# Performance work log

Hardware: AMD Instinct MI355X
Metric: run time of the kernel (lower is better)

Reference implementation:

```python
import jax, jax.numpy as jnp
import numpy as np


def setup_inputs() -> dict:
    key = jax.random.key(0)
    k1, k2 = jax.random.split(key)
    B, S, D, T = 64, 512, 768, 384
    hidden_states = jax.random.normal(k1, (B, S, D), dtype=jnp.float32)
    # sorted per-row segment ids: each subtoken belongs to a token index in [0, T)
    segment_ids = jnp.sort(jax.random.randint(k2, (B, S), 0, T), axis=-1)
    return {"hidden_states": hidden_states, "segment_ids": segment_ids, "num_tokens": T}


def reference(hidden_states, segment_ids, num_tokens):
    # Segment-mean of subtoken embeddings into token embeddings.
    # Equivalent to the original running-mean loop:
    #   prev + (next - prev) / n_subtoken_per_token  == mean over the group.
    B, S, D = hidden_states.shape
    # flatten batch into segment ids so one segment_sum handles all sequences
    flat_ids = (segment_ids + jnp.arange(B, dtype=segment_ids.dtype)[:, None] * num_tokens).reshape(-1)
    sums = jax.ops.segment_sum(hidden_states.reshape(-1, D), flat_ids,
                               num_segments=B * num_tokens)  # [B*T, D]
    counts = jax.ops.segment_sum(jnp.ones((B * S,), dtype=hidden_states.dtype), flat_ids,
                                 num_segments=B * num_tokens)  # [B*T]
    # tokens with no subtokens stay zero (original initializes with zeros)
    means = sums / jnp.maximum(counts, 1.0)[:, None]
    return means.reshape(B, num_tokens, D)
```

## Files before the change

kernel.cpp:

```cpp
#include <hip/hip_runtime.h>


__global__ void bounds_kernel(const int* __restrict__ seg,
                              const int* __restrict__ num_tokens_p,
                              int* __restrict__ start,
                              int BS_total,
                              int BT) {
  const int T = num_tokens_p[0];
  const int B = BT / T;
  const int S = BS_total / B;
  int idx = blockIdx.x * blockDim.x + threadIdx.x;
  if (idx >= BS_total) return;
  const int b = idx / S;
  const int s = idx - b * S;
  const int cur = seg[idx];
  const int prev = (s == 0) ? -1 : seg[idx - 1];
  int* __restrict__ row = start + (size_t)b * (T + 1);
  for (int t = prev + 1; t <= cur; ++t) row[t] = s;
  if (s == S - 1) {
    for (int t = cur + 1; t <= T; ++t) row[t] = S;
  }
}

__global__ void __launch_bounds__(192) seg_mean_kernel(
    const float* __restrict__ hs,
    const int* __restrict__ start,
    const int* __restrict__ num_tokens_p,
    float* __restrict__ out,
    int BS_total,
    int D) {
  const int T = num_tokens_p[0];
  const int BT = gridDim.x;
  const int S = (int)(((long long)BS_total * T) / BT);
  const int b = blockIdx.x / T;
  const int t = blockIdx.x - b * T;

  const int* __restrict__ srow = start + (size_t)b * (T + 1) + t;
  const int lo = srow[0];
  const int hi = srow[1];
  const int cnt = hi - lo;

  const int d4 = threadIdx.x;
  const int rowstride4 = D >> 2;

  const float4* __restrict__ p =
      (const float4*)(hs + ((size_t)b * S + lo) * D) + d4;

  float4 acc = make_float4(0.f, 0.f, 0.f, 0.f);
  for (int s = 0; s < cnt; ++s) {
    float4 v = p[(size_t)s * rowstride4];
    acc.x += v.x; acc.y += v.y; acc.z += v.z; acc.w += v.w;
  }

  const float inv = (cnt > 0) ? (1.0f / (float)cnt) : 0.0f;
  float4 o = make_float4(acc.x * inv, acc.y * inv, acc.z * inv, acc.w * inv);

  ((float4*)(out + (size_t)blockIdx.x * D))[d4] = o;
}

__global__ void __launch_bounds__(192) seg_mean_search_kernel(
    const float* __restrict__ hs,
    const int* __restrict__ seg,
    const int* __restrict__ num_tokens_p,
    float* __restrict__ out,
    int BS_total,
    int D) {
  const int T = num_tokens_p[0];
  const int BT = gridDim.x;
  const int S = (int)(((long long)BS_total * T) / BT);
  const int b = blockIdx.x / T;
  const int t = blockIdx.x - b * T;
  const int* __restrict__ row = seg + (size_t)b * S;

  int lo = 0, n = S;
  while (n > 0) {
    int half = n >> 1;
    int mid = lo + half;
    if (row[mid] < t) { lo = mid + 1; n -= half + 1; } else { n = half; }
  }
  int hi = lo; n = S - lo;
  while (n > 0) {
    int half = n >> 1;
    int mid = hi + half;
    if (row[mid] < t + 1) { hi = mid + 1; n -= half + 1; } else { n = half; }
  }
  const int cnt = hi - lo;

  const int d4 = threadIdx.x;
  const int rowstride4 = D >> 2;
  const float4* __restrict__ p =
      (const float4*)(hs + ((size_t)b * S + lo) * D) + d4;

  float4 acc = make_float4(0.f, 0.f, 0.f, 0.f);
  for (int s = 0; s < cnt; ++s) {
    float4 v = p[(size_t)s * rowstride4];
    acc.x += v.x; acc.y += v.y; acc.z += v.z; acc.w += v.w;
  }
  const float inv = (cnt > 0) ? (1.0f / (float)cnt) : 0.0f;
  float4 o = make_float4(acc.x * inv, acc.y * inv, acc.z * inv, acc.w * inv);
  ((float4*)(out + (size_t)blockIdx.x * D))[d4] = o;
}

extern "C" void kernel_launch(void* const* d_in, const int* in_sizes, int n_in,
                              void* d_out, int out_size, void* d_ws, size_t ws_size,
                              hipStream_t stream) {
  const float* hs = (const float*)d_in[0];
  const int* seg = (const int*)d_in[1];
  const int* num_tokens_p = (const int*)d_in[2];
  float* out = (float*)d_out;

  const int BS_total = in_sizes[1];
  const int D = in_sizes[0] / in_sizes[1];
  const int BT = out_size / D;

  const size_t ws_needed = (size_t)4 * ((size_t)BT + (size_t)BS_total);

  if (ws_size >= ws_needed) {
    int* start = (int*)d_ws;
    const int threads1 = 256;
    const int grid1 = (BS_total + threads1 - 1) / threads1;
    hipLaunchKernelGGL(bounds_kernel, dim3(grid1), dim3(threads1), 0, stream,
                       seg, num_tokens_p, start, BS_total, BT);
    hipLaunchKernelGGL(seg_mean_kernel, dim3(BT), dim3(D / 4), 0, stream,
                       hs, start, num_tokens_p, out, BS_total, D);
  } else {
    hipLaunchKernelGGL(seg_mean_search_kernel, dim3(BT), dim3(D / 4), 0, stream,
                       hs, seg, num_tokens_p, out, BS_total, D);
  }
}
```

Before: 172.1 us.

## Fuse segment bounds computation into mean kernel with 8 tokens per block

Replaces the separate bounds kernel and per-token mean kernel with a single kernel in which each block handles 8 consecutive tokens. Each block scans its row of segment ids in shared memory, using ballots and atomics to find its start offset and per-token counts, then averages the subtoken rows for each token. This removes one kernel launch and the workspace round trip. In exchange every block rereads a full 512-entry segment row, the grid shrinks by a factor of 8, and each block's token loop runs serially.

Result: slower. 183.1 us (+6.4%).

```diff
diff --git a/kernel.cpp b/kernel.cpp
--- a/kernel.cpp
+++ b/kernel.cpp
@@ -1,104 +1,120 @@
 #include <hip/hip_runtime.h>
 
 
-__global__ void bounds_kernel(const int* __restrict__ seg,
-                              const int* __restrict__ num_tokens_p,
-                              int* __restrict__ start,
-                              int BS_total,
-                              int BT) {
+#define TPB_TOKENS 8
+
+__global__ void __launch_bounds__(192) seg_mean_fused(
+    const float* __restrict__ hs,
+    const int*   __restrict__ seg,
+    const int*   __restrict__ num_tokens_p,
+    float*       __restrict__ out,
+    int BS_total,
+    int BT,
+    int D) {
   const int T = num_tokens_p[0];
   const int B = BT / T;
   const int S = BS_total / B;
-  int idx = blockIdx.x * blockDim.x + threadIdx.x;
-  if (idx >= BS_total) return;
-  const int b = idx / S;
-  const int s = idx - b * S;
-  const int cur = seg[idx];
-  const int prev = (s == 0) ? -1 : seg[idx - 1];
-  int* __restrict__ row = start + (size_t)b * (T + 1);
-  for (int t = prev + 1; t <= cur; ++t) row[t] = s;
-  if (s == S - 1) {
-    for (int t = cur + 1; t <= T; ++t) row[t] = S;
-  }
-}
 
-__global__ void __launch_bounds__(192) seg_mean_kernel(
-    const float* __restrict__ hs,
-    const int* __restrict__ start,
-    const int* __restrict__ num_tokens_p,
-    float* __restrict__ out,
-    int BS_total,
-    int D) {
-  const int T = num_tokens_p[0];
-  const int BT = gridDim.x;
-  const int S = (int)(((long long)BS_total * T) / BT);
-  const int b = blockIdx.x / T;
-  const int t = blockIdx.x - b * T;
+  const int g0 = blockIdx.x * TPB_TOKENS;
+  if (g0 >= BT) return;
+  const int gEnd = min(g0 + TPB_TOKENS, BT);
 
-  const int* __restrict__ srow = start + (size_t)b * (T + 1) + t;
-  const int lo = srow[0];
-  const int hi = srow[1];
-  const int cnt = hi - lo;
-
-  const int d4 = threadIdx.x;
+  const int tid  = threadIdx.x;
+  const int lane = tid & 63;
+  const int d4   = tid;
   const int rowstride4 = D >> 2;
 
-  const float4* __restrict__ p =
-      (const float4*)(hs + ((size_t)b * S + lo) * D) + d4;
+  __shared__ int sh_bounds[TPB_TOKENS + 1];
+  __shared__ int sh_bins[TPB_TOKENS];
+  __shared__ int sh_base;
+  __shared__ int sh_hi;
 
-  float4 acc = make_float4(0.f, 0.f, 0.f, 0.f);
-  for (int s = 0; s < cnt; ++s) {
-    float4 v = p[(size_t)s * rowstride4];
-    acc.x += v.x; acc.y += v.y; acc.z += v.z; acc.w += v.w;
+  const int b0    = g0 / T;
+  const int bLast = (gEnd - 1) / T;
+
+  if (b0 == bLast) {
+    const int t0   = g0 - b0 * T;
+    const int nTok = gEnd - g0;
+
+    if (tid < TPB_TOKENS) sh_bins[tid] = 0;
+    if (tid == 0) sh_base = 0;
+    __syncthreads();
+
+    const int* __restrict__ srow = seg + (size_t)b0 * S;
+    for (int s = tid; s < S; s += blockDim.x) {
+      const int v = srow[s];
+      unsigned long long m = __ballot(v < t0);
+      if (lane == 0) atomicAdd(&sh_base, __popcll(m));
+      const int rel = v - t0;
+      if (rel >= 0 && rel < nTok) atomicAdd(&sh_bins[rel], 1);
+    }
+    __syncthreads();
+
+    if (tid == 0) {
+      int acc = sh_base;
+      sh_bounds[0] = acc;
+      #pragma unroll
+      for (int j = 0; j < TPB_TOKENS; ++j) {
+        acc += sh_bins[j];
+        sh_bounds[j + 1] = acc;
+      }
+    }
+    __syncthreads();
+
+    const float4* __restrict__ base =
+        (const float4*)(hs + (size_t)b0 * S * D) + d4;
+
+    for (int j = 0; j < nTok; ++j) {
+      const int lo  = sh_bounds[j];
+      const int cnt = sh_bounds[j + 1] - lo;
+
+      float4 acc = make_float4(0.f, 0.f, 0.f, 0.f);
+      const float4* __restrict__ p = base + (size_t)lo * rowstride4;
+      for (int s = 0; s < cnt; ++s) {
+        float4 v = p[(size_t)s * rowstride4];
+        acc.x += v.x; acc.y += v.y; acc.z += v.z; acc.w += v.w;
+      }
+      const float inv = (cnt > 0) ? (1.0f / (float)cnt) : 0.0f;
+      float4 o = make_float4(acc.x * inv, acc.y * inv, acc.z * inv, acc.w * inv);
+      ((float4*)(out + (size_t)(g0 + j) * D))[d4] = o;
+    }
+  } else {
+    for (int g = g0; g < gEnd; ++g) {
+      const int b = g / T;
+      const int t = g - b * T;
+
+      if (tid == 0) { sh_base = 0; sh_hi = 0; }
+      __syncthreads();
+
+      const int* __restrict__ srow = seg + (size_t)b * S;
+      for (int s = tid; s < S; s += blockDim.x) {
+        const int v = srow[s];
+        unsigned long long mlo = __ballot(v < t);
+        unsigned long long mhi = __ballot(v < t + 1);
+        if (lane == 0) {
+          atomicAdd(&sh_base, __popcll(mlo));
+          atomicAdd(&sh_hi,   __popcll(mhi));
+        }
+      }
+      __syncthreads();
+
+      const int lo  = sh_base;
+      const int cnt = sh_hi - lo;
+
+      float4 acc = make_float4(0.f, 0.f, 0.f, 0.f);
+      const float4* __restrict__ p =
+          (const float4*)(hs + ((size_t)b * S + lo) * D) + d4;
+      for (int s = 0; s < cnt; ++s) {
+        float4 v = p[(size_t)s * rowstride4];
+        acc.x += v.x; acc.y += v.y; acc.z += v.z; acc.w += v.w;
+      }
+      const float inv = (cnt > 0) ? (1.0f / (float)cnt) : 0.0f;
+      float4 o = make_float4(acc.x * inv, acc.y * inv, acc.z * inv, acc.w * inv);
+      ((float4*)(out + (size_t)g * D))[d4] = o;
+
+      __syncthreads();
+    }
   }
-
-  const float inv = (cnt > 0) ? (1.0f / (float)cnt) : 0.0f;
-  float4 o = make_float4(acc.x * inv, acc.y * inv, acc.z * inv, acc.w * inv);
-
-  ((float4*)(out + (size_t)blockIdx.x * D))[d4] = o;
-}
-
-__global__ void __launch_bounds__(192) seg_mean_search_kernel(
-    const float* __restrict__ hs,
-    const int* __restrict__ seg,
-    const int* __restrict__ num_tokens_p,
-    float* __restrict__ out,
-    int BS_total,
-    int D) {
-  const int T = num_tokens_p[0];
-  const int BT = gridDim.x;
-  const int S = (int)(((long long)BS_total * T) / BT);
-  const int b = blockIdx.x / T;
-  const int t = blockIdx.x - b * T;
-  const int* __restrict__ row = seg + (size_t)b * S;
-
-  int lo = 0, n = S;
-  while (n > 0) {
-    int half = n >> 1;
-    int mid = lo + half;
-    if (row[mid] < t) { lo = mid + 1; n -= half + 1; } else { n = half; }
-  }
-  int hi = lo; n = S - lo;
-  while (n > 0) {
-    int half = n >> 1;
-    int mid = hi + half;
-    if (row[mid] < t + 1) { hi = mid + 1; n -= half + 1; } else { n = half; }
-  }
-  const int cnt = hi - lo;
-
-  const int d4 = threadIdx.x;
-  const int rowstride4 = D >> 2;
-  const float4* __restrict__ p =
-      (const float4*)(hs + ((size_t)b * S + lo) * D) + d4;
-
-  float4 acc = make_float4(0.f, 0.f, 0.f, 0.f);
-  for (int s = 0; s < cnt; ++s) {
-    float4 v = p[(size_t)s * rowstride4];
-    acc.x += v.x; acc.y += v.y; acc.z += v.z; acc.w += v.w;
-  }
-  const float inv = (cnt > 0) ? (1.0f / (float)cnt) : 0.0f;
-  float4 o = make_float4(acc.x * inv, acc.y * inv, acc.z * inv, acc.w * inv);
-  ((float4*)(out + (size_t)blockIdx.x * D))[d4] = o;
 }
 
 extern "C" void kernel_launch(void* const* d_in, const int* in_sizes, int n_in,
@@ -113,18 +129,7 @@
   const int D = in_sizes[0] / in_sizes[1];
   const int BT = out_size / D;
 
-  const size_t ws_needed = (size_t)4 * ((size_t)BT + (size_t)BS_total);
-
-  if (ws_size >= ws_needed) {
-    int* start = (int*)d_ws;
-    const int threads1 = 256;
-    const int grid1 = (BS_total + threads1 - 1) / threads1;
-    hipLaunchKernelGGL(bounds_kernel, dim3(grid1), dim3(threads1), 0, stream,
-                       seg, num_tokens_p, start, BS_total, BT);
-    hipLaunchKernelGGL(seg_mean_kernel, dim3(BT), dim3(D / 4), 0, stream,
-                       hs, start, num_tokens_p, out, BS_total, D);
-  } else {
-    hipLaunchKernelGGL(seg_mean_search_kernel, dim3(BT), dim3(D / 4), 0, stream,
-                       hs, seg, num_tokens_p, out, BS_total, D);
-  }
+  const int grid = (BT + TPB_TOKENS - 1) / TPB_TOKENS;
+  hipLaunchKernelGGL(seg_mean_fused, dim3(grid), dim3(D / 4), 0, stream,
+                     hs, seg, num_tokens_p, out, BS_total, BT, D);
 }
```

## Map one wave per token with grid-stride loop and prefetched absolute bounds

Applied to the files above, without the earlier changes.

The bounds kernel now writes absolute (start,end) row pairs per token instead of per-row start offsets, so the mean kernel needs a single int2 load. The mean kernel assigns one 64-lane wave per token, with each lane handling three float4 columns for D=768. It uses a capped grid-stride loop that prefetches the next token's bounds. This is meant to cut per-block launch and scheduling overhead and raise memory-level parallelism per thread. The cost is fewer resident blocks and a specialised path that only applies when D is 768.

New measurement: 178.0 us. 1.03x slower.

```diff
diff --git a/kernel.cpp b/kernel.cpp
--- a/kernel.cpp
+++ b/kernel.cpp
@@ -1,61 +1,110 @@
 #include <hip/hip_runtime.h>
 
 
-__global__ void bounds_kernel(const int* __restrict__ seg,
-                              const int* __restrict__ num_tokens_p,
-                              int* __restrict__ start,
-                              int BS_total,
-                              int BT) {
+#define PHASE2_WAVES 4
+
+__global__ void bounds_pairs_kernel(const int* __restrict__ seg,
+                                    const int* __restrict__ num_tokens_p,
+                                    int2* __restrict__ pairs,
+                                    int BS_total,
+                                    int BT) {
   const int T = num_tokens_p[0];
   const int B = BT / T;
   const int S = BS_total / B;
-  int idx = blockIdx.x * blockDim.x + threadIdx.x;
+  const int idx = blockIdx.x * blockDim.x + threadIdx.x;
   if (idx >= BS_total) return;
   const int b = idx / S;
   const int s = idx - b * S;
   const int cur = seg[idx];
   const int prev = (s == 0) ? -1 : seg[idx - 1];
-  int* __restrict__ row = start + (size_t)b * (T + 1);
-  for (int t = prev + 1; t <= cur; ++t) row[t] = s;
+  int2* __restrict__ prow = pairs + (size_t)b * T;
+
+  for (int t = prev + 1; t <= cur; ++t) {
+    prow[t].x = idx;
+    if (t > 0) prow[t - 1].y = idx;
+  }
   if (s == S - 1) {
-    for (int t = cur + 1; t <= T; ++t) row[t] = S;
+    const int end = b * S + S;
+    for (int t = cur + 1; t <= T; ++t) {
+      if (t < T) prow[t].x = end;
+      prow[t - 1].y = end;
+    }
   }
 }
 
-__global__ void __launch_bounds__(192) seg_mean_kernel(
+__global__ void __launch_bounds__(64 * PHASE2_WAVES) seg_mean_d768(
     const float* __restrict__ hs,
-    const int* __restrict__ start,
-    const int* __restrict__ num_tokens_p,
-    float* __restrict__ out,
-    int BS_total,
-    int D) {
-  const int T = num_tokens_p[0];
-  const int BT = gridDim.x;
-  const int S = (int)(((long long)BS_total * T) / BT);
-  const int b = blockIdx.x / T;
-  const int t = blockIdx.x - b * T;
+    const int2*  __restrict__ pairs,
+    float*       __restrict__ out,
+    int BT) {
+  const int wave = threadIdx.x >> 6;
+  const int lane = threadIdx.x & 63;
+  const int gstride = gridDim.x * PHASE2_WAVES;
 
-  const int* __restrict__ srow = start + (size_t)b * (T + 1) + t;
-  const int lo = srow[0];
-  const int hi = srow[1];
-  const int cnt = hi - lo;
+  int g = blockIdx.x * PHASE2_WAVES + wave;
+  if (g >= BT) return;
+  int2 lh = pairs[g];
 
-  const int d4 = threadIdx.x;
-  const int rowstride4 = D >> 2;
+  while (true) {
+    const int gn = g + gstride;
+    int2 lh_next;
+    if (gn < BT) lh_next = pairs[gn];
 
-  const float4* __restrict__ p =
-      (const float4*)(hs + ((size_t)b * S + lo) * D) + d4;
+    const int cnt = lh.y - lh.x;
+    const float4* __restrict__ p =
+        (const float4*)hs + (size_t)lh.x * 192 + lane;
 
-  float4 acc = make_float4(0.f, 0.f, 0.f, 0.f);
-  for (int s = 0; s < cnt; ++s) {
-    float4 v = p[(size_t)s * rowstride4];
-    acc.x += v.x; acc.y += v.y; acc.z += v.z; acc.w += v.w;
+    float4 a0 = make_float4(0.f, 0.f, 0.f, 0.f);
+    float4 a1 = a0, a2 = a0;
+    for (int r = 0; r < cnt; ++r) {
+      float4 v0 = p[0];
+      float4 v1 = p[64];
+      float4 v2 = p[128];
+      a0.x += v0.x; a0.y += v0.y; a0.z += v0.z; a0.w += v0.w;
+      a1.x += v1.x; a1.y += v1.y; a1.z += v1.z; a1.w += v1.w;
+      a2.x += v2.x; a2.y += v2.y; a2.z += v2.z; a2.w += v2.w;
+      p += 192;
+    }
+
+    const float inv = (cnt > 0) ? (1.0f / (float)cnt) : 0.0f;
+    float4* __restrict__ q = (float4*)out + (size_t)g * 192 + lane;
+    q[0]   = make_float4(a0.x * inv, a0.y * inv, a0.z * inv, a0.w * inv);
+    q[64]  = make_float4(a1.x * inv, a1.y * inv, a1.z * inv, a1.w * inv);
+    q[128] = make_float4(a2.x * inv, a2.y * inv, a2.z * inv, a2.w * inv);
+
+    if (gn >= BT) break;
+    g = gn;
+    lh = lh_next;
   }
+}
 
-  const float inv = (cnt > 0) ? (1.0f / (float)cnt) : 0.0f;
-  float4 o = make_float4(acc.x * inv, acc.y * inv, acc.z * inv, acc.w * inv);
+__global__ void __launch_bounds__(64 * PHASE2_WAVES) seg_mean_generic(
+    const float* __restrict__ hs,
+    const int2*  __restrict__ pairs,
+    float*       __restrict__ out,
+    int BT,
+    int dv4) {
+  const int wave = threadIdx.x >> 6;
+  const int lane = threadIdx.x & 63;
+  const int gstride = gridDim.x * PHASE2_WAVES;
 
-  ((float4*)(out + (size_t)blockIdx.x * D))[d4] = o;
+  for (int g = blockIdx.x * PHASE2_WAVES + wave; g < BT; g += gstride) {
+    const int2 lh = pairs[g];
+    const int cnt = lh.y - lh.x;
+    const float inv = (cnt > 0) ? (1.0f / (float)cnt) : 0.0f;
+
+    for (int c = lane; c < dv4; c += 64) {
+      const float4* __restrict__ p = (const float4*)hs + (size_t)lh.x * dv4 + c;
+      float4 acc = make_float4(0.f, 0.f, 0.f, 0.f);
+      for (int r = 0; r < cnt; ++r) {
+        float4 v = *p;
+        acc.x += v.x; acc.y += v.y; acc.z += v.z; acc.w += v.w;
+        p += dv4;
+      }
+      ((float4*)(out + (size_t)g * (dv4 * 4)))[c] =
+          make_float4(acc.x * inv, acc.y * inv, acc.z * inv, acc.w * inv);
+    }
+  }
 }
 
 __global__ void __launch_bounds__(192) seg_mean_search_kernel(
@@ -113,16 +162,27 @@
   const int D = in_sizes[0] / in_sizes[1];
   const int BT = out_size / D;
 
-  const size_t ws_needed = (size_t)4 * ((size_t)BT + (size_t)BS_total);
+  const size_t ws_needed = (size_t)8 * (size_t)BT;
 
   if (ws_size >= ws_needed) {
-    int* start = (int*)d_ws;
+    int2* pairs = (int2*)d_ws;
+
     const int threads1 = 256;
     const int grid1 = (BS_total + threads1 - 1) / threads1;
-    hipLaunchKernelGGL(bounds_kernel, dim3(grid1), dim3(threads1), 0, stream,
-                       seg, num_tokens_p, start, BS_total, BT);
-    hipLaunchKernelGGL(seg_mean_kernel, dim3(BT), dim3(D / 4), 0, stream,
-                       hs, start, num_tokens_p, out, BS_total, D);
+    hipLaunchKernelGGL(bounds_pairs_kernel, dim3(grid1), dim3(threads1), 0, stream,
+                       seg, num_tokens_p, pairs, BS_total, BT);
+
+    const int maxBlocks = 2048;
+    const int needBlocks = (BT + PHASE2_WAVES - 1) / PHASE2_WAVES;
+    const int grid2 = (needBlocks < maxBlocks) ? needBlocks : maxBlocks;
+
+    if (D == 768) {
+      hipLaunchKernelGGL(seg_mean_d768, dim3(grid2), dim3(64 * PHASE2_WAVES), 0,
+                         stream, hs, pairs, out, BT);
+    } else {
+      hipLaunchKernelGGL(seg_mean_generic, dim3(grid2), dim3(64 * PHASE2_WAVES), 0,
+                         stream, hs, pairs, out, BT, D / 4);
+    }
   } else {
     hipLaunchKernelGGL(seg_mean_search_kernel, dim3(BT), dim3(D / 4), 0, stream,
                        hs, seg, num_tokens_p, out, BS_total, D);
```
